# Optimization experiments

Hardware: AMD Instinct MI355X
Metric: run time of the kernel (lower is better)

The kernel has to match this reference:

```python
import jax, jax.numpy as jnp
import numpy as np

B, DIM, N = 16, 512, 4096


def setup_inputs() -> dict:
    key = jax.random.key(0)
    kx, kq, kk, kv = jax.random.split(key, 4)
    scale = 1.0 / np.sqrt(DIM)
    return {
        "x": jax.random.normal(kx, (B, DIM, N), dtype=jnp.float32),
        "Wq": jax.random.normal(kq, (DIM, DIM), dtype=jnp.float32) * scale,
        "Wk": jax.random.normal(kk, (DIM, DIM), dtype=jnp.float32) * scale,
        "Wv": jax.random.normal(kv, (DIM, DIM), dtype=jnp.float32) * scale,
    }


def reference(x, Wq, Wk, Wv):
    # x: [B, dim, N]; 1x1 conv over channel dim == matmul with [dim_out, dim_in]
    dim = x.shape[1]
    temperature = jnp.sqrt(jnp.asarray(dim, dtype=x.dtype))
    q = jnp.einsum("dc,bcn->bdn", Wq, x)  # [B, dim, N]
    k = jnp.einsum("dc,bcn->bdn", Wk, x)
    v = jnp.einsum("dc,bcn->bdn", Wv, x)
    # channel attention: contract over N points -> [B, dim, dim]
    attn = jnp.einsum("bdn,ben->bde", q / temperature, k)
    attn = jax.nn.softmax(attn, axis=-1)
    out = jnp.einsum("bde,ben->bdn", attn, v)  # [B, dim, N]
    return out
```

## Files before the change

### kernel.cpp

```cpp
#include <hip/hip_runtime.h>
#include <hip/hip_bf16.h>
#include <math.h>

#define DIMC 512
#define NPT  4096
#define BATCH 16
#define KSPLIT 4

typedef __bf16 bf16x4 __attribute__((ext_vector_type(4)));
typedef __bf16 bf16x8 __attribute__((ext_vector_type(8)));
typedef float  f32x4  __attribute__((ext_vector_type(4)));

typedef const __attribute__((address_space(1))) unsigned int guint;
typedef __attribute__((address_space(3))) unsigned int luint;

__device__ inline void gl_lds16(const void* g, void* l) {
  __builtin_amdgcn_global_load_lds((guint*)g, (luint*)l, 16, 0, 0);
}

__global__ __launch_bounds__(256, 4) void gram_split(
    const __bf16* __restrict__ xb, float* __restrict__ Gp)
{
  static const int TI[10] = {0,0,0,0,1,1,1,2,2,3};
  static const int TJ[10] = {0,1,2,3,1,2,3,2,3,3};
  const int id = blockIdx.x;
  const int xcd = id & 7, slot = id >> 3;
  const int g = slot / 10, t = slot % 10;
  const int pair = xcd + 8 * g;
  const int b = pair >> 2, s = pair & 3;
  const int m0 = TI[t] * 128, n0 = TJ[t] * 128;

  const __bf16* A = xb + (long)b * DIMC * NPT;
  float* C = Gp + (long)pair * DIMC * DIMC;

  __shared__ alignas(16) __bf16 As[128 * 32];
  __shared__ alignas(16) __bf16 Bs[128 * 32];

  const int tid  = threadIdx.x;
  const int wave = tid >> 6, lane = tid & 63;
  const int wr = wave >> 1, wc = wave & 1;
  const int q = lane >> 4, p = lane & 15;
  const int r4 = lane >> 2;
  const int koff = (lane & 3) * 8;

  f32x4 acc[4][4];
#pragma unroll
  for (int i = 0; i < 4; ++i)
#pragma unroll
    for (int j = 0; j < 4; ++j) acc[i][j] = (f32x4){0.f, 0.f, 0.f, 0.f};

  const __bf16* gA = A + (long)m0 * NPT;
  const __bf16* gB = A + (long)n0 * NPT;
  const int kbeg = s * (NPT / KSPLIT), kend = kbeg + NPT / KSPLIT;

  for (int k0 = kbeg; k0 < kend; k0 += 32) {
    __syncthreads();
#pragma unroll
    for (int h = 0; h < 2; ++h) {
      const int chunk = wave + h * 4;
      gl_lds16(gA + (long)(chunk * 16 + r4) * NPT + k0 + koff, &As[chunk * 512]);
      gl_lds16(gB + (long)(chunk * 16 + r4) * NPT + k0 + koff, &Bs[chunk * 512]);
    }
    __syncthreads();

    bf16x8 af[4], bfv[4];
#pragma unroll
    for (int i = 0; i < 4; ++i)
      af[i] = ((const bf16x8*)As)[(wr * 64 + i * 16 + p) * 4 + q];
#pragma unroll
    for (int j = 0; j < 4; ++j)
      bfv[j] = ((const bf16x8*)Bs)[(wc * 64 + j * 16 + p) * 4 + q];
#pragma unroll
    for (int i = 0; i < 4; ++i)
#pragma unroll
      for (int j = 0; j < 4; ++j)
        acc[i][j] = __builtin_amdgcn_mfma_f32_16x16x32_bf16(af[i], bfv[j], acc[i][j], 0, 0, 0);
  }

#pragma unroll
  for (int i = 0; i < 4; ++i) {
    const int row = m0 + wr * 64 + i * 16 + q * 4;
#pragma unroll
    for (int j = 0; j < 4; ++j) {
      const int col = n0 + wc * 64 + j * 16 + p;
#pragma unroll
      for (int r = 0; r < 4; ++r)
        C[(long)(row + r) * DIMC + col] = acc[i][j][r];
    }
  }
}

__global__ __launch_bounds__(256) void gram_reduce_mirror(
    const float* __restrict__ Gp, __bf16* __restrict__ Gh, __bf16* __restrict__ Gl)
{
  const int bid = blockIdx.x;
  const int b = bid / 36;
  int rem = bid % 36, I = 0;
  while (rem >= 8 - I) { rem -= 8 - I; ++I; }
  const int J = I + rem;

  __shared__ float T[64][65];
  const int tid = threadIdx.x;
  const int r = tid >> 2, c0 = (tid & 3) * 16;

  float v[16];
#pragma unroll
  for (int e = 0; e < 16; ++e) v[e] = 0.f;
#pragma unroll
  for (int s = 0; s < KSPLIT; ++s) {
    const float* src = Gp + (long)(b * KSPLIT + s) * DIMC * DIMC
                          + (long)(I * 64 + r) * DIMC + J * 64 + c0;
#pragma unroll
    for (int q = 0; q < 4; ++q) {
      float4 t4 = ((const float4*)src)[q];
      v[q * 4 + 0] += t4.x; v[q * 4 + 1] += t4.y;
      v[q * 4 + 2] += t4.z; v[q * 4 + 3] += t4.w;
    }
  }

  const long gbase = (long)b * DIMC * DIMC;
#pragma unroll
  for (int q = 0; q < 4; ++q) {
    bf16x4 h, l;
#pragma unroll
    for (int e = 0; e < 4; ++e) {
      float f = v[q * 4 + e];
      __bf16 hh = (__bf16)f;
      h[e] = hh; l[e] = (__bf16)(f - (float)hh);
    }
    const long o = gbase + (long)(I * 64 + r) * DIMC + J * 64 + c0 + q * 4;
    *(bf16x4*)(Gh + o) = h;
    *(bf16x4*)(Gl + o) = l;
  }
#pragma unroll
  for (int e = 0; e < 16; ++e) T[r][c0 + e] = v[e];
  __syncthreads();
  if (I != J) {
#pragma unroll
    for (int q = 0; q < 4; ++q) {
      bf16x4 h, l;
#pragma unroll
      for (int e = 0; e < 4; ++e) {
        float f = T[c0 + q * 4 + e][r];
        __bf16 hh = (__bf16)f;
        h[e] = hh; l[e] = (__bf16)(f - (float)hh);
      }
      const long o = gbase + (long)(J * 64 + r) * DIMC + I * 64 + c0 + q * 4;
      *(bf16x4*)(Gh + o) = h;
      *(bf16x4*)(Gl + o) = l;
    }
  }
}

template <bool SPLIT_OUT>
__global__ __launch_bounds__(256, 4) void gemm3_nt(
    const __bf16* __restrict__ Ah, const __bf16* __restrict__ Al,
    const __bf16* __restrict__ Bh, const __bf16* __restrict__ Bl,
    float* __restrict__ Cf, __bf16* __restrict__ Ch, __bf16* __restrict__ Cl,
    int K, long sA, long sB, long sC, float alpha)
{
  const int b = blockIdx.z;
  Ah += (long)b * sA;  Al += (long)b * sA;
  Bh += (long)b * sB;  Bl += (long)b * sB;
  const int m0 = blockIdx.y * 64, n0 = blockIdx.x * 128;

  __shared__ alignas(16) __bf16 sAh[64 * 32],  sAl[64 * 32];
  __shared__ alignas(16) __bf16 sBh[128 * 32], sBl[128 * 32];

  const int tid  = threadIdx.x;
  const int wave = tid >> 6, lane = tid & 63;
  const int wr = wave >> 1, wc = wave & 1;
  const int q = lane >> 4, p = lane & 15;
  const int r4 = lane >> 2;
  const int koff = (lane & 3) * 8;

  f32x4 acc[2][4];
#pragma unroll
  for (int i = 0; i < 2; ++i)
#pragma unroll
    for (int j = 0; j < 4; ++j) acc[i][j] = (f32x4){0.f, 0.f, 0.f, 0.f};

  const long arow = (long)(m0 + wave * 16 + r4) * K + koff;

  for (int k0 = 0; k0 < K; k0 += 32) {
    __syncthreads();
    gl_lds16(Ah + arow + k0, &sAh[wave * 512]);
    gl_lds16(Al + arow + k0, &sAl[wave * 512]);
#pragma unroll
    for (int h = 0; h < 2; ++h) {
      const int chunk = wave + h * 4;
      const long brow = (long)(n0 + chunk * 16 + r4) * K + koff + k0;
      gl_lds16(Bh + brow, &sBh[chunk * 512]);
      gl_lds16(Bl + brow, &sBl[chunk * 512]);
    }
    __syncthreads();

    bf16x8 fah[2], fal[2], fbh[4], fbl[4];
#pragma unroll
    for (int i = 0; i < 2; ++i) {
      const int idx = (wr * 32 + i * 16 + p) * 4 + q;
      fah[i] = ((const bf16x8*)sAh)[idx];
      fal[i] = ((const bf16x8*)sAl)[idx];
    }
#pragma unroll
    for (int j = 0; j < 4; ++j) {
      const int idx = (wc * 64 + j * 16 + p) * 4 + q;
      fbh[j] = ((const bf16x8*)sBh)[idx];
      fbl[j] = ((const bf16x8*)sBl)[idx];
    }
#pragma unroll
    for (int i = 0; i < 2; ++i)
#pragma unroll
      for (int j = 0; j < 4; ++j) {
        acc[i][j] = __builtin_amdgcn_mfma_f32_16x16x32_bf16(fah[i], fbh[j], acc[i][j], 0, 0, 0);
        acc[i][j] = __builtin_amdgcn_mfma_f32_16x16x32_bf16(fah[i], fbl[j], acc[i][j], 0, 0, 0);
        acc[i][j] = __builtin_amdgcn_mfma_f32_16x16x32_bf16(fal[i], fbh[j], acc[i][j], 0, 0, 0);
      }
  }

#pragma unroll
  for (int i = 0; i < 2; ++i) {
    const int row = m0 + wr * 32 + i * 16 + q * 4;
#pragma unroll
    for (int j = 0; j < 4; ++j) {
      const int col = n0 + wc * 64 + j * 16 + p;
#pragma unroll
      for (int r = 0; r < 4; ++r) {
        const float f = acc[i][j][r] * alpha;
        const long o = (long)b * sC + (long)(row + r) * DIMC + col;
        if (SPLIT_OUT) {
          __bf16 hh = (__bf16)f;
          Ch[o] = hh;
          Cl[o] = (__bf16)(f - (float)hh);
        } else {
          Cf[o] = f;
        }
      }
    }
  }
}

__global__ __launch_bounds__(256, 4) void gemm_nt64x128(
    const __bf16* __restrict__ A, const __bf16* __restrict__ B,
    __bf16* __restrict__ C, int K, long sA, long sB, long sC)
{
  const int b = blockIdx.z;
  A += (long)b * sA;  B += (long)b * sB;  C += (long)b * sC;
  const int m0 = blockIdx.y * 64, n0 = blockIdx.x * 128;

  __shared__ alignas(16) __bf16 As[64 * 32];
  __shared__ alignas(16) __bf16 Bs[128 * 32];

  const int tid  = threadIdx.x;
  const int wave = tid >> 6, lane = tid & 63;
  const int wr = wave >> 1, wc = wave & 1;
  const int q = lane >> 4, p = lane & 15;
  const int r4 = lane >> 2;
  const int koff = (lane & 3) * 8;

  f32x4 acc[2][4];
#pragma unroll
  for (int i = 0; i < 2; ++i)
#pragma unroll
    for (int j = 0; j < 4; ++j) acc[i][j] = (f32x4){0.f, 0.f, 0.f, 0.f};

  const long arow = (long)(m0 + wave * 16 + r4) * K + koff;

  for (int k0 = 0; k0 < K; k0 += 32) {
    __syncthreads();
    gl_lds16(A + arow + k0, &As[wave * 512]);
#pragma unroll
    for (int h = 0; h < 2; ++h) {
      const int chunk = wave + h * 4;
      gl_lds16(B + (long)(n0 + chunk * 16 + r4) * K + koff + k0, &Bs[chunk * 512]);
    }
    __syncthreads();

    bf16x8 af[2], bfv[4];
#pragma unroll
    for (int i = 0; i < 2; ++i)
      af[i] = ((const bf16x8*)As)[(wr * 32 + i * 16 + p) * 4 + q];
#pragma unroll
    for (int j = 0; j < 4; ++j)
      bfv[j] = ((const bf16x8*)Bs)[(wc * 64 + j * 16 + p) * 4 + q];
#pragma unroll
    for (int i = 0; i < 2; ++i)
#pragma unroll
      for (int j = 0; j < 4; ++j)
        acc[i][j] = __builtin_amdgcn_mfma_f32_16x16x32_bf16(af[i], bfv[j], acc[i][j], 0, 0, 0);
  }

#pragma unroll
  for (int i = 0; i < 2; ++i) {
    const int row = m0 + wr * 32 + i * 16 + q * 4;
#pragma unroll
    for (int j = 0; j < 4; ++j) {
      const int col = n0 + wc * 64 + j * 16 + p;
#pragma unroll
      for (int r = 0; r < 4; ++r)
        C[(long)(row + r) * DIMC + col] = (__bf16)acc[i][j][r];
    }
  }
}

__global__ __launch_bounds__(256, 2) void gemm_final(
    const __bf16* __restrict__ Mm, const __bf16* __restrict__ xb,
    float* __restrict__ out)
{
  const int id = blockIdx.x;
  const int xcd = id & 7, slot = id >> 3;
  const int g = slot >> 7, tile = slot & 127;
  const int b = xcd + 8 * g;
  const int m0 = (tile >> 5) * 128, n0 = (tile & 31) * 128;

  const __bf16* A = Mm + (long)b * DIMC * DIMC;
  const __bf16* B = xb + (long)b * DIMC * NPT;
  float* C = out + (long)b * DIMC * NPT;
  const int K = DIMC;

  __shared__ alignas(16) __bf16 As[128 * 32];
  __shared__ alignas(16) unsigned int Bs[128 * 18];

  const int tid  = threadIdx.x;
  const int wave = tid >> 6, lane = tid & 63;
  const int wr = wave >> 1, wc = wave & 1;
  const int q = lane >> 4, p = lane & 15;
  const int r4 = lane >> 2;
  const int koff = (lane & 3) * 8;

  const int ng = tid & 31;
  const int cq = tid >> 5;

  f32x4 acc[4][4];
#pragma unroll
  for (int i = 0; i < 4; ++i)
#pragma unroll
    for (int j = 0; j < 4; ++j) acc[i][j] = (f32x4){0.f, 0.f, 0.f, 0.f};

  const __bf16* gA = A + (long)m0 * K;

  for (int k0 = 0; k0 < K; k0 += 32) {
    __syncthreads();
#pragma unroll
    for (int h = 0; h < 2; ++h) {
      const int chunk = wave + h * 4;
      gl_lds16(gA + (long)(chunk * 16 + r4) * K + k0 + koff, &As[chunk * 512]);
    }
    uint2 rd[4];
#pragma unroll
    for (int r = 0; r < 4; ++r)
      rd[r] = *(const uint2*)(B + (long)(k0 + cq * 4 + r) * NPT + n0 + ng * 4);
#pragma unroll
    for (int nn = 0; nn < 4; ++nn) {
      const unsigned int s0 = (nn < 2) ? rd[0].x : rd[0].y;
      const unsigned int s1 = (nn < 2) ? rd[1].x : rd[1].y;
      const unsigned int s2 = (nn < 2) ? rd[2].x : rd[2].y;
      const unsigned int s3 = (nn < 2) ? rd[3].x : rd[3].y;
      unsigned int o01, o23;
      if (nn & 1) {
        o01 = (s0 >> 16) | (s1 & 0xffff0000u);
        o23 = (s2 >> 16) | (s3 & 0xffff0000u);
      } else {
        o01 = (s0 & 0xffffu) | (s1 << 16);
        o23 = (s2 & 0xffffu) | (s3 << 16);
      }
      uint2 o; o.x = o01; o.y = o23;
      *(uint2*)&Bs[(ng * 4 + nn) * 18 + cq * 2] = o;
    }
    __syncthreads();

    bf16x8 af[4], bfv[4];
#pragma unroll
    for (int i = 0; i < 4; ++i)
      af[i] = ((const bf16x8*)As)[(wr * 64 + i * 16 + p) * 4 + q];
#pragma unroll
    for (int j = 0; j < 4; ++j) {
      const unsigned int* bp = &Bs[(wc * 64 + j * 16 + p) * 18 + q * 4];
      const uint2 lo = *(const uint2*)bp;
      const uint2 hi = *(const uint2*)(bp + 2);
      union { uint4 u; bf16x8 v; } cvt;
      cvt.u.x = lo.x; cvt.u.y = lo.y; cvt.u.z = hi.x; cvt.u.w = hi.y;
      bfv[j] = cvt.v;
    }
#pragma unroll
    for (int i = 0; i < 4; ++i)
#pragma unroll
      for (int j = 0; j < 4; ++j)
        acc[i][j] = __builtin_amdgcn_mfma_f32_16x16x32_bf16(af[i], bfv[j], acc[i][j], 0, 0, 0);
  }

#pragma unroll
  for (int i = 0; i < 4; ++i) {
    const int row = m0 + wr * 64 + i * 16 + q * 4;
#pragma unroll
    for (int j = 0; j < 4; ++j) {
      const int col = n0 + wc * 64 + j * 16 + p;
#pragma unroll
      for (int r = 0; r < 4; ++r)
        C[(long)(row + r) * NPT + col] = acc[i][j][r];
    }
  }
}

__global__ __launch_bounds__(256) void convert_x(
    const float* __restrict__ x, __bf16* __restrict__ xb)
{
  const long total8 = (long)BATCH * DIMC * NPT / 8;
  const long stride = (long)gridDim.x * 256;
  for (long i = blockIdx.x * 256 + threadIdx.x; i < total8; i += stride) {
    const f32x4 a = ((const f32x4*)x)[2 * i];
    const f32x4 b = ((const f32x4*)x)[2 * i + 1];
    bf16x8 o;
    o[0] = (__bf16)a[0]; o[1] = (__bf16)a[1];
    o[2] = (__bf16)a[2]; o[3] = (__bf16)a[3];
    o[4] = (__bf16)b[0]; o[5] = (__bf16)b[1];
    o[6] = (__bf16)b[2]; o[7] = (__bf16)b[3];
    ((bf16x8*)xb)[i] = o;
  }
}

__global__ __launch_bounds__(256) void softmax_rows(
    const float* __restrict__ S, __bf16* __restrict__ P)
{
  const int row = blockIdx.x * 4 + (threadIdx.x >> 6);
  const int lane = threadIdx.x & 63;
  const float4* s4 = (const float4*)(S + (long)row * DIMC);
  float4 a = s4[lane * 2], b = s4[lane * 2 + 1];
  float v[8] = {a.x, a.y, a.z, a.w, b.x, b.y, b.z, b.w};
  float m = v[0];
#pragma unroll
  for (int i = 1; i < 8; ++i) m = fmaxf(m, v[i]);
#pragma unroll
  for (int off = 32; off > 0; off >>= 1) m = fmaxf(m, __shfl_xor(m, off));
  float e[8], sum = 0.f;
#pragma unroll
  for (int i = 0; i < 8; ++i) { e[i] = expf(v[i] - m); sum += e[i]; }
#pragma unroll
  for (int off = 32; off > 0; off >>= 1) sum += __shfl_xor(sum, off);
  const float inv = 1.0f / sum;
  bf16x8 o;
#pragma unroll
  for (int i = 0; i < 8; ++i) o[i] = (__bf16)(e[i] * inv);
  ((bf16x8*)(P + (long)row * DIMC))[lane] = o;
}

__global__ __launch_bounds__(256) void make_w(
    const float* __restrict__ Wq, const float* __restrict__ Wk,
    const float* __restrict__ Wv,
    __bf16* __restrict__ Wqh, __bf16* __restrict__ Wql,
    __bf16* __restrict__ Wkh, __bf16* __restrict__ Wkl,
    __bf16* __restrict__ WvT)
{
  const int i = blockIdx.x * 256 + threadIdx.x;
  float q = Wq[i];
  __bf16 qh = (__bf16)q; Wqh[i] = qh; Wql[i] = (__bf16)(q - (float)qh);
  float k = Wk[i];
  __bf16 kh = (__bf16)k; Wkh[i] = kh; Wkl[i] = (__bf16)(k - (float)kh);
  const int e = i >> 9, c = i & 511;
  WvT[(long)c * DIMC + e] = (__bf16)Wv[i];
}

extern "C" void kernel_launch(void* const* d_in, const int* in_sizes, int n_in,
                              void* d_out, int out_size, void* d_ws, size_t ws_size,
                              hipStream_t stream)
{
  const float* x  = (const float*)d_in[0];
  const float* Wq = (const float*)d_in[1];
  const float* Wk = (const float*)d_in[2];
  const float* Wv = (const float*)d_in[3];
  float* out = (float*)d_out;

  char* ws = (char*)d_ws;
  size_t off = 0;
  auto alloc = [&](size_t bytes) -> void* {
    void* p = ws + off;
    off += (bytes + 255) & ~(size_t)255;
    return p;
  };
  const long s2 = (long)DIMC * DIMC;

  __bf16* xb  = (__bf16*)alloc((size_t)BATCH * DIMC * NPT * 2);
  float*  Gp  = (float*) alloc((size_t)KSPLIT * BATCH * s2 * 4);
  __bf16* Gh  = (__bf16*)alloc((size_t)BATCH * s2 * 2);
  __bf16* Gl  = (__bf16*)alloc((size_t)BATCH * s2 * 2);
  __bf16* Hh  = (__bf16*)alloc((size_t)BATCH * s2 * 2);
  __bf16* Hl  = (__bf16*)alloc((size_t)BATCH * s2 * 2);
  __bf16* Wqh = (__bf16*)alloc((size_t)s2 * 2);
  __bf16* Wql = (__bf16*)alloc((size_t)s2 * 2);
  __bf16* Wkh = (__bf16*)alloc((size_t)s2 * 2);
  __bf16* Wkl = (__bf16*)alloc((size_t)s2 * 2);
  __bf16* WvT = (__bf16*)alloc((size_t)s2 * 2);
  float*  S  = (float*)Gp;
  __bf16* P  = Gl;
  __bf16* Mm = Gh;

  make_w<<<DIMC * DIMC / 256, 256, 0, stream>>>(Wq, Wk, Wv, Wqh, Wql, Wkh, Wkl, WvT);
  convert_x<<<2048, 256, 0, stream>>>(x, xb);
  gram_split<<<640, 256, 0, stream>>>(xb, Gp);
  gram_reduce_mirror<<<BATCH * 36, 256, 0, stream>>>(Gp, Gh, Gl);
  gemm3_nt<true><<<dim3(4, 8, BATCH), 256, 0, stream>>>(
      Wqh, Wql, Gh, Gl, (float*)nullptr, Hh, Hl, DIMC, 0L, s2, s2, 1.0f);
  gemm3_nt<false><<<dim3(4, 8, BATCH), 256, 0, stream>>>(
      Hh, Hl, Wkh, Wkl, S, (__bf16*)nullptr, (__bf16*)nullptr,
      DIMC, s2, 0L, s2, 0.044194173824159216f);
  softmax_rows<<<BATCH * DIMC / 4, 256, 0, stream>>>(S, P);
  gemm_nt64x128<<<dim3(4, 8, BATCH), 256, 0, stream>>>(
      P, WvT, Mm, DIMC, s2, 0L, s2);
  gemm_final<<<2048, 256, 0, stream>>>(Mm, xb, out);
}
```

Measured before the change: 394.3 us.

## Fuse softmax into P·WvT GEMM, merge prep kernels, raise gemm_final occupancy

```diff
diff --git a/kernel.cpp b/kernel.cpp
--- a/kernel.cpp
+++ b/kernel.cpp
@@ -240,15 +240,16 @@
   }
 }
 
-__global__ __launch_bounds__(256, 4) void gemm_nt64x128(
-    const __bf16* __restrict__ A, const __bf16* __restrict__ B,
-    __bf16* __restrict__ C, int K, long sA, long sB, long sC)
+__global__ __launch_bounds__(256, 2) void softmax_pv(
+    const float* __restrict__ S, const __bf16* __restrict__ WvT,
+    __bf16* __restrict__ Mm)
 {
   const int b = blockIdx.z;
-  A += (long)b * sA;  B += (long)b * sB;  C += (long)b * sC;
   const int m0 = blockIdx.y * 64, n0 = blockIdx.x * 128;
-
-  __shared__ alignas(16) __bf16 As[64 * 32];
+  const float* Sb = S + (long)b * DIMC * DIMC;
+  __bf16* C = Mm + (long)b * DIMC * DIMC;
+
+  __shared__ alignas(16) __bf16 Ps[64 * 512];
   __shared__ alignas(16) __bf16 Bs[128 * 32];
 
   const int tid  = threadIdx.x;
@@ -258,28 +259,52 @@
   const int r4 = lane >> 2;
   const int koff = (lane & 3) * 8;
 
+#pragma unroll 1
+  for (int it = 0; it < 16; ++it) {
+    const int row = wave * 16 + it;
+    const float* sr = Sb + (long)(m0 + row) * DIMC + lane * 8;
+    const f32x4 a = *(const f32x4*)sr;
+    const f32x4 bb = *(const f32x4*)(sr + 4);
+    float v[8] = {a[0], a[1], a[2], a[3], bb[0], bb[1], bb[2], bb[3]};
+    float m = v[0];
+#pragma unroll
+    for (int i = 1; i < 8; ++i) m = fmaxf(m, v[i]);
+#pragma unroll
+    for (int off = 32; off > 0; off >>= 1) m = fmaxf(m, __shfl_xor(m, off));
+    float e[8], sum = 0.f;
+#pragma unroll
+    for (int i = 0; i < 8; ++i) { e[i] = expf(v[i] - m); sum += e[i]; }
+#pragma unroll
+    for (int off = 32; off > 0; off >>= 1) sum += __shfl_xor(sum, off);
+    const float inv = 1.0f / sum;
+    bf16x8 o;
+#pragma unroll
+    for (int i = 0; i < 8; ++i) o[i] = (__bf16)(e[i] * inv);
+    ((bf16x8*)Ps)[row * 64 + (lane ^ (row & 7))] = o;
+  }
+  __syncthreads();
+
   f32x4 acc[2][4];
 #pragma unroll
   for (int i = 0; i < 2; ++i)
 #pragma unroll
     for (int j = 0; j < 4; ++j) acc[i][j] = (f32x4){0.f, 0.f, 0.f, 0.f};
 
-  const long arow = (long)(m0 + wave * 16 + r4) * K + koff;
-
-  for (int k0 = 0; k0 < K; k0 += 32) {
-    __syncthreads();
-    gl_lds16(A + arow + k0, &As[wave * 512]);
+  for (int k0 = 0; k0 < DIMC; k0 += 32) {
+    if (k0) __syncthreads();
 #pragma unroll
     for (int h = 0; h < 2; ++h) {
       const int chunk = wave + h * 4;
-      gl_lds16(B + (long)(n0 + chunk * 16 + r4) * K + koff + k0, &Bs[chunk * 512]);
+      gl_lds16(WvT + (long)(n0 + chunk * 16 + r4) * DIMC + koff + k0, &Bs[chunk * 512]);
     }
     __syncthreads();
 
     bf16x8 af[2], bfv[4];
 #pragma unroll
-    for (int i = 0; i < 2; ++i)
-      af[i] = ((const bf16x8*)As)[(wr * 32 + i * 16 + p) * 4 + q];
+    for (int i = 0; i < 2; ++i) {
+      const int row = wr * 32 + i * 16 + p;
+      af[i] = ((const bf16x8*)Ps)[row * 64 + (((k0 >> 3) + q) ^ (row & 7))];
+    }
 #pragma unroll
     for (int j = 0; j < 4; ++j)
       bfv[j] = ((const bf16x8*)Bs)[(wc * 64 + j * 16 + p) * 4 + q];
@@ -303,7 +328,7 @@
   }
 }
 
-__global__ __launch_bounds__(256, 2) void gemm_final(
+__global__ __launch_bounds__(256, 3) void gemm_final(
     const __bf16* __restrict__ Mm, const __bf16* __restrict__ xb,
     float* __restrict__ out)
 {
@@ -402,12 +427,27 @@
   }
 }
 
-__global__ __launch_bounds__(256) void convert_x(
-    const float* __restrict__ x, __bf16* __restrict__ xb)
-{
+__global__ __launch_bounds__(256) void prep(
+    const float* __restrict__ x, __bf16* __restrict__ xb,
+    const float* __restrict__ Wq, const float* __restrict__ Wk,
+    const float* __restrict__ Wv,
+    __bf16* __restrict__ Wqh, __bf16* __restrict__ Wql,
+    __bf16* __restrict__ Wkh, __bf16* __restrict__ Wkl,
+    __bf16* __restrict__ WvT)
+{
+  if (blockIdx.x < 1024) {
+    const int i = blockIdx.x * 256 + threadIdx.x;
+    float q = Wq[i];
+    __bf16 qh = (__bf16)q; Wqh[i] = qh; Wql[i] = (__bf16)(q - (float)qh);
+    float k = Wk[i];
+    __bf16 kh = (__bf16)k; Wkh[i] = kh; Wkl[i] = (__bf16)(k - (float)kh);
+    const int e = i >> 9, c = i & 511;
+    WvT[(long)c * DIMC + e] = (__bf16)Wv[i];
+    return;
+  }
   const long total8 = (long)BATCH * DIMC * NPT / 8;
-  const long stride = (long)gridDim.x * 256;
-  for (long i = blockIdx.x * 256 + threadIdx.x; i < total8; i += stride) {
+  const long stride = (long)(gridDim.x - 1024) * 256;
+  for (long i = (long)(blockIdx.x - 1024) * 256 + threadIdx.x; i < total8; i += stride) {
     const f32x4 a = ((const f32x4*)x)[2 * i];
     const f32x4 b = ((const f32x4*)x)[2 * i + 1];
     bf16x8 o;
@@ -417,47 +457,6 @@
     o[6] = (__bf16)b[2]; o[7] = (__bf16)b[3];
     ((bf16x8*)xb)[i] = o;
   }
-}
-
-__global__ __launch_bounds__(256) void softmax_rows(
-    const float* __restrict__ S, __bf16* __restrict__ P)
-{
-  const int row = blockIdx.x * 4 + (threadIdx.x >> 6);
-  const int lane = threadIdx.x & 63;
-  const float4* s4 = (const float4*)(S + (long)row * DIMC);
-  float4 a = s4[lane * 2], b = s4[lane * 2 + 1];
-  float v[8] = {a.x, a.y, a.z, a.w, b.x, b.y, b.z, b.w};
-  float m = v[0];
-#pragma unroll
-  for (int i = 1; i < 8; ++i) m = fmaxf(m, v[i]);
-#pragma unroll
-  for (int off = 32; off > 0; off >>= 1) m = fmaxf(m, __shfl_xor(m, off));
-  float e[8], sum = 0.f;
-#pragma unroll
-  for (int i = 0; i < 8; ++i) { e[i] = expf(v[i] - m); sum += e[i]; }
-#pragma unroll
-  for (int off = 32; off > 0; off >>= 1) sum += __shfl_xor(sum, off);
-  const float inv = 1.0f / sum;
-  bf16x8 o;
-#pragma unroll
-  for (int i = 0; i < 8; ++i) o[i] = (__bf16)(e[i] * inv);
-  ((bf16x8*)(P + (long)row * DIMC))[lane] = o;
-}
-
-__global__ __launch_bounds__(256) void make_w(
-    const float* __restrict__ Wq, const float* __restrict__ Wk,
-    const float* __restrict__ Wv,
-    __bf16* __restrict__ Wqh, __bf16* __restrict__ Wql,
-    __bf16* __restrict__ Wkh, __bf16* __restrict__ Wkl,
-    __bf16* __restrict__ WvT)
-{
-  const int i = blockIdx.x * 256 + threadIdx.x;
-  float q = Wq[i];
-  __bf16 qh = (__bf16)q; Wqh[i] = qh; Wql[i] = (__bf16)(q - (float)qh);
-  float k = Wk[i];
-  __bf16 kh = (__bf16)k; Wkh[i] = kh; Wkl[i] = (__bf16)(k - (float)kh);
-  const int e = i >> 9, c = i & 511;
-  WvT[(long)c * DIMC + e] = (__bf16)Wv[i];
 }
 
 extern "C" void kernel_launch(void* const* d_in, const int* in_sizes, int n_in,
@@ -491,11 +490,9 @@
   __bf16* Wkl = (__bf16*)alloc((size_t)s2 * 2);
   __bf16* WvT = (__bf16*)alloc((size_t)s2 * 2);
   float*  S  = (float*)Gp;
-  __bf16* P  = Gl;
   __bf16* Mm = Gh;
 
-  make_w<<<DIMC * DIMC / 256, 256, 0, stream>>>(Wq, Wk, Wv, Wqh, Wql, Wkh, Wkl, WvT);
-  convert_x<<<2048, 256, 0, stream>>>(x, xb);
+  prep<<<3072, 256, 0, stream>>>(x, xb, Wq, Wk, Wv, Wqh, Wql, Wkh, Wkl, WvT);
   gram_split<<<640, 256, 0, stream>>>(xb, Gp);
   gram_reduce_mirror<<<BATCH * 36, 256, 0, stream>>>(Gp, Gh, Gl);
   gemm3_nt<true><<<dim3(4, 8, BATCH), 256, 0, stream>>>(
@@ -503,8 +500,6 @@
   gemm3_nt<false><<<dim3(4, 8, BATCH), 256, 0, stream>>>(
       Hh, Hl, Wkh, Wkl, S, (__bf16*)nullptr, (__bf16*)nullptr,
       DIMC, s2, 0L, s2, 0.044194173824159216f);
-  softmax_rows<<<BATCH * DIMC / 4, 256, 0, stream>>>(S, P);
-  gemm_nt64x128<<<dim3(4, 8, BATCH), 256, 0, stream>>>(
-      P, WvT, Mm, DIMC, s2, 0L, s2);
+  softmax_pv<<<dim3(4, 8, BATCH), 256, 0, stream>>>(S, WvT, Mm);
   gemm_final<<<2048, 256, 0, stream>>>(Mm, xb, out);
 }
```

Result: no change. 399.1 us (+1.2%).
